# Performance work log

Measured on AMD Instinct MI355X. Metric: run time of the kernel, lower is better.

Reference implementation:

```python
import jax, jax.numpy as jnp
import numpy as np

TOTAL_LABELS = 81
MAX_TOTAL_SIZE = 200
SCORE_THRESHOLD = 0.7
IOU_THRESHOLD = 0.5  # tf.image.combined_non_max_suppression default
VARIANCES = jnp.array([0.1, 0.1, 0.2, 0.2], dtype=jnp.float32)
B, N = 4, 1500


def setup_inputs() -> dict:
    key = jax.random.key(0)
    k1, k2, k3, k4, k5 = jax.random.split(key, 5)
    # valid normalized rois (y1,x1,y2,x2) with y1<y2, x1<x2
    ctr = jax.random.uniform(k1, (B, N, 2), minval=0.2, maxval=0.8)
    sz = jax.random.uniform(k2, (B, N, 2), minval=0.05, maxval=0.3)
    roi_bboxes = jnp.concatenate([ctr - 0.5 * sz, ctr + 0.5 * sz], axis=-1).astype(jnp.float32)
    pred_deltas = (0.5 * jax.random.normal(k3, (B, N, TOTAL_LABELS * 4))).astype(jnp.float32)
    # peaked probabilities so a realistic fraction clears score_threshold=0.7
    logits = 4.0 * jax.random.normal(k4, (B, N, TOTAL_LABELS))
    pred_label_probs = jax.nn.softmax(logits, axis=-1).astype(jnp.float32)
    return {"roi_bboxes": roi_bboxes, "pred_deltas": pred_deltas,
            "pred_label_probs": pred_label_probs}


def delta_to_bbox(anchors, deltas):
    # anchors/deltas: [..., 4]; anchors are (y1,x1,y2,x2), deltas (dy,dx,dh,dw)
    h = anchors[..., 2] - anchors[..., 0]
    w = anchors[..., 3] - anchors[..., 1]
    cy = anchors[..., 0] + 0.5 * h
    cx = anchors[..., 1] + 0.5 * w
    bh = jnp.exp(deltas[..., 2]) * h
    bw = jnp.exp(deltas[..., 3]) * w
    bcy = deltas[..., 0] * h + cy
    bcx = deltas[..., 1] * w + cx
    y1 = bcy - 0.5 * bh
    x1 = bcx - 0.5 * bw
    return jnp.stack([y1, x1, y1 + bh, x1 + bw], axis=-1)


def _iou_one_vs_all(box, boxes):
    yy1 = jnp.maximum(box[0], boxes[:, 0])
    xx1 = jnp.maximum(box[1], boxes[:, 1])
    yy2 = jnp.minimum(box[2], boxes[:, 2])
    xx2 = jnp.minimum(box[3], boxes[:, 3])
    inter = jnp.maximum(yy2 - yy1, 0.0) * jnp.maximum(xx2 - xx1, 0.0)
    a1 = (box[2] - box[0]) * (box[3] - box[1])
    a2 = (boxes[:, 2] - boxes[:, 0]) * (boxes[:, 3] - boxes[:, 1])
    union = a1 + a2 - inter
    return jnp.where(union > 0, inter / union, 0.0)


def _greedy_nms(boxes, scores):
    # boxes [N,4], scores [N] -> sel idx [K] (-1 invalid), sel score [K]
    def step(scores_c, _):
        j = jnp.argmax(scores_c)
        s = scores_c[j]
        valid = s > SCORE_THRESHOLD
        iou = _iou_one_vs_all(boxes[j], boxes)
        new_scores = jnp.where(valid & (iou > IOU_THRESHOLD), -jnp.inf, scores_c)
        return new_scores, (jnp.where(valid, j, -1).astype(jnp.int32),
                            jnp.where(valid, s, 0.0))
    _, (idx, sc) = jax.lax.scan(step, scores, None, length=MAX_TOTAL_SIZE)
    return idx, sc


def _decoder_forward(roi_bboxes, pred_deltas, pred_label_probs):
    b, n, L = pred_label_probs.shape
    deltas = pred_deltas.reshape(b, n, L, 4) * VARIANCES
    rois = jnp.broadcast_to(roi_bboxes[:, :, None, :], (b, n, L, 4))
    pred_bboxes = delta_to_bbox(rois, deltas)              # [B,N,L,4]
    labels_map = jnp.argmax(pred_label_probs, axis=-1, keepdims=True)
    scores = jnp.where(labels_map != 0, pred_label_probs, 0.0)  # zero bg boxes
    boxes_cl = jnp.transpose(pred_bboxes, (0, 2, 1, 3))    # [B,L,N,4]
    scores_cl = jnp.transpose(scores, (0, 2, 1))           # [B,L,N]
    idx, sc = jax.vmap(jax.vmap(_greedy_nms))(boxes_cl, scores_cl)  # [B,L,K]
    K = MAX_TOTAL_SIZE
    sel_boxes = jnp.take_along_axis(boxes_cl, jnp.maximum(idx, 0)[..., None], axis=2)
    valid = (idx >= 0)[..., None]
    sel_boxes = jnp.where(valid, jnp.clip(sel_boxes, 0.0, 1.0), 0.0)  # clip_boxes=True
    cls = jnp.broadcast_to(jnp.arange(L, dtype=jnp.float32)[None, :, None], (b, L, K))
    cls = jnp.where(idx >= 0, cls, 0.0)
    flat_scores = sc.reshape(b, L * K)
    flat_boxes = sel_boxes.reshape(b, L * K, 4)
    flat_cls = cls.reshape(b, L * K)
    final_scores, top_i = jax.lax.top_k(flat_scores, MAX_TOTAL_SIZE)
    final_bboxes = jnp.take_along_axis(flat_boxes, top_i[..., None], axis=1)
    final_labels = jnp.take_along_axis(flat_cls, top_i, axis=1)
    return final_bboxes, final_labels, final_scores


def reference(roi_bboxes, pred_deltas, pred_label_probs):
    return _decoder_forward(roi_bboxes, pred_deltas, pred_label_probs)
```

## Files before the change

### kernel.cpp

```cpp
#include <hip/hip_runtime.h>
#include <math.h>

#define NCLS 81
#define KMAX 200
#define NMAX 1536
#define SORT_CAP 2048


__global__ __launch_bounds__(64) void row_scan(
    const float* __restrict__ rois,
    const float* __restrict__ deltas,
    const float* __restrict__ probs,
    int* __restrict__ cand_cls,
    float* __restrict__ cand_sc,
    float4* __restrict__ cand_box,
    int BN) {
  __shared__ float s_p[64 * NCLS];
  const int lane = threadIdx.x;
  const int row0 = blockIdx.x * 64;

  if (row0 + 64 <= BN) {
    const float4* src4 = (const float4*)(probs + (size_t)row0 * NCLS);
    float4* dst4 = (float4*)s_p;
#pragma unroll
    for (int it = 0; it < 21; ++it) {
      const int idx = it * 64 + lane;
      if (idx < 1296) dst4[idx] = src4[idx];
    }
  } else {
    const int tot = (BN - row0) * NCLS;
    const float* src = probs + (size_t)row0 * NCLS;
    for (int i = lane; i < tot; i += 64) s_p[i] = src[i];
  }
  __syncthreads();

  const int row = row0 + lane;
  if (row >= BN) return;
  const float* pr = s_p + lane * NCLS;
  float maxv = pr[0];
  int arg = 0;
#pragma unroll
  for (int k = 1; k < NCLS; ++k) {
    const float v = pr[k];
    if (v > maxv) { maxv = v; arg = k; }
  }
  const bool cand = (maxv > 0.7f) && (arg != 0);
  cand_cls[row] = cand ? arg : -1;
  cand_sc[row] = maxv;
  if (cand) {
    const float* r = rois + (size_t)row * 4;
    const float ay1 = r[0], ax1 = r[1], ay2 = r[2], ax2 = r[3];
    const float h = ay2 - ay1, w = ax2 - ax1;
    const float cy = ay1 + 0.5f * h, cx = ax1 + 0.5f * w;
    const float* d = deltas + (size_t)row * (NCLS * 4) + arg * 4;
    const float bh  = expf(d[2] * 0.2f) * h;
    const float bw  = expf(d[3] * 0.2f) * w;
    const float bcy = d[0] * 0.1f * h + cy;
    const float bcx = d[1] * 0.1f * w + cx;
    const float y1 = bcy - 0.5f * bh, x1 = bcx - 0.5f * bw;
    cand_box[row] = make_float4(y1, x1, y1 + bh, x1 + bw);
  }
}

__device__ __forceinline__ void nms_body(
    const float* __restrict__ cand_sc, const float4* __restrict__ cand_box,
    float* __restrict__ entries, int* __restrict__ counts,
    int N, int b, int l, int bl, int lane, int m,
    int* s_idx, float* s_score, float (*s_box)[4],
    int* s_sel, float* s_sel_score) {
  for (int i = lane; i < m; i += 64) {
    const int n = s_idx[i];
    s_score[i] = cand_sc[b * N + n];
    const float4 bx = cand_box[b * N + n];
    s_box[i][0] = bx.x; s_box[i][1] = bx.y;
    s_box[i][2] = bx.z; s_box[i][3] = bx.w;
  }
  __syncthreads();

  int kept = 0;
  while (kept < KMAX) {
    float best = -1.0f;
    int bi = -1;
    for (int i = lane; i < m; i += 64) {
      const float s = s_score[i];
      if (s > best) { best = s; bi = i; }
    }
    for (int off = 32; off > 0; off >>= 1) {
      const float ob = __shfl_down(best, off);
      const int   oi = __shfl_down(bi, off);
      if (ob > best || (ob == best && (unsigned)oi < (unsigned)bi)) {
        best = ob; bi = oi;
      }
    }
    best = __shfl(best, 0);
    bi   = __shfl(bi, 0);
    if (best <= 0.7f) break;

    if (lane == 0) { s_sel[kept] = bi; s_sel_score[kept] = best; }

    const float by1 = s_box[bi][0], bx1 = s_box[bi][1];
    const float by2 = s_box[bi][2], bx2 = s_box[bi][3];
    const float a1 = (by2 - by1) * (bx2 - bx1);
    for (int i = lane; i < m; i += 64) {
      const float ty1 = s_box[i][0], tx1 = s_box[i][1];
      const float ty2 = s_box[i][2], tx2 = s_box[i][3];
      const float yy1 = fmaxf(by1, ty1), xx1 = fmaxf(bx1, tx1);
      const float yy2 = fminf(by2, ty2), xx2 = fminf(bx2, tx2);
      const float inter = fmaxf(yy2 - yy1, 0.0f) * fmaxf(xx2 - xx1, 0.0f);
      const float a2  = (ty2 - ty1) * (tx2 - tx1);
      const float uni = a1 + a2 - inter;
      const float iou = (uni > 0.0f) ? (inter / uni) : 0.0f;
      if (iou > 0.5f) s_score[i] = -INFINITY;
    }
    kept++;
    __syncthreads();
  }
  __syncthreads();

  if (lane == 0) counts[bl] = kept;
  float* ebase = entries + (size_t)bl * KMAX * 8;
  for (int i = lane; i < kept; i += 64) {
    float* e = ebase + (size_t)i * 8;
    const int ci = s_sel[i];
    e[0] = s_sel_score[i];
    e[1] = fminf(fmaxf(s_box[ci][0], 0.0f), 1.0f);
    e[2] = fminf(fmaxf(s_box[ci][1], 0.0f), 1.0f);
    e[3] = fminf(fmaxf(s_box[ci][2], 0.0f), 1.0f);
    e[4] = fminf(fmaxf(s_box[ci][3], 0.0f), 1.0f);
  }
}

template <int N>
__global__ __launch_bounds__(64) void nms_per_class(
    const int* __restrict__ cand_cls, const float* __restrict__ cand_sc,
    const float4* __restrict__ cand_box, float* __restrict__ entries,
    int* __restrict__ counts) {
  constexpr int ITERS = (N + 63) / 64;
  const int bl = blockIdx.x;
  const int b  = bl / NCLS;
  const int l  = bl % NCLS;
  const int lane = threadIdx.x;
  if (l == 0) { if (lane == 0) counts[bl] = 0; return; }

  __shared__ int   s_idx[NMAX];
  __shared__ float s_score[NMAX];
  __shared__ float s_box[NMAX][4];
  __shared__ int   s_sel[KMAX];
  __shared__ float s_sel_score[KMAX];

  int cv[ITERS];
#pragma unroll
  for (int it = 0; it < ITERS; ++it) {
    const int n = it * 64 + lane;
    cv[it] = (n < N) ? cand_cls[b * N + n] : -1;
  }
  int m = 0;
#pragma unroll
  for (int it = 0; it < ITERS; ++it) {
    const bool cand = (cv[it] == l);
    const unsigned long long mask = __ballot(cand);
    if (cand)
      s_idx[m + __popcll(mask & ((1ull << lane) - 1ull))] = it * 64 + lane;
    m += __popcll(mask);
  }
  __syncthreads();

  nms_body(cand_sc, cand_box, entries, counts, N, b, l, bl, lane, m,
           s_idx, s_score, s_box, s_sel, s_sel_score);
}

__global__ __launch_bounds__(64) void nms_per_class_rt(
    const int* __restrict__ cand_cls, const float* __restrict__ cand_sc,
    const float4* __restrict__ cand_box, float* __restrict__ entries,
    int* __restrict__ counts, int N) {
  const int bl = blockIdx.x;
  const int b  = bl / NCLS;
  const int l  = bl % NCLS;
  const int lane = threadIdx.x;
  if (l == 0) { if (lane == 0) counts[bl] = 0; return; }

  __shared__ int   s_idx[NMAX];
  __shared__ float s_score[NMAX];
  __shared__ float s_box[NMAX][4];
  __shared__ int   s_sel[KMAX];
  __shared__ float s_sel_score[KMAX];

  int m = 0;
  for (int n0 = 0; n0 < N; n0 += 64) {
    const int n = n0 + lane;
    const bool cand = (n < N) && (cand_cls[b * N + n] == l);
    const unsigned long long mask = __ballot(cand);
    if (cand)
      s_idx[m + __popcll(mask & ((1ull << lane) - 1ull))] = n;
    m += __popcll(mask);
  }
  __syncthreads();

  nms_body(cand_sc, cand_box, entries, counts, N, b, l, bl, lane, m,
           s_idx, s_score, s_box, s_sel, s_sel_score);
}

__global__ __launch_bounds__(1024) void topk_per_batch(
    const float* __restrict__ entries,
    const int* __restrict__ counts,
    float* __restrict__ out, int B) {
  const int b   = blockIdx.x;
  const int tid = threadIdx.x;

  __shared__ int s_cnt[NCLS];
  __shared__ int s_off[NCLS];
  __shared__ int s_total, s_M;
  __shared__ unsigned long long s_key[SORT_CAP];

  if (tid < NCLS) s_cnt[tid] = counts[b * NCLS + tid];
  __syncthreads();
  if (tid == 0) {
    int acc = 0;
    for (int l = 0; l < NCLS; ++l) { s_off[l] = acc; acc += s_cnt[l]; }
    s_total = acc;
    int M = 64;
    while (M < acc) M <<= 1;
    s_M = M;
  }
  __syncthreads();
  const int c = s_total;
  const int M = s_M;

  for (int i = tid; i < M; i += 1024) s_key[i] = 0ull;
  __syncthreads();
  for (int j = tid; j < NCLS * KMAX; j += 1024) {
    const int l = j / KMAX, k = j - l * KMAX;
    if (k < s_cnt[l]) {
      const float sc = entries[((size_t)(b * NCLS + l) * KMAX + k) * 8];
      const unsigned sb = __float_as_uint(sc);
      s_key[s_off[l] + k] =
          ((unsigned long long)sb << 32) |
          (unsigned long long)(0xFFFFFFFFu - (unsigned)(l * KMAX + k));
    }
  }
  __syncthreads();

  for (int kk = 2; kk <= M; kk <<= 1) {
    for (int j2 = kk >> 1; j2 > 0; j2 >>= 1) {
      for (int i = tid; i < M; i += 1024) {
        const int ixj = i ^ j2;
        if (ixj > i) {
          const bool up = ((i & kk) == 0);
          const unsigned long long a = s_key[i], bb = s_key[ixj];
          const bool sw = up ? (a < bb) : (a > bb);
          if (sw) { s_key[i] = bb; s_key[ixj] = a; }
        }
      }
      __syncthreads();
    }
  }

  if (tid < KMAX) {
    float sc = 0.0f, lb = 0.0f, b0 = 0.0f, b1 = 0.0f, b2 = 0.0f, b3 = 0.0f;
    if (tid < c) {
      const unsigned long long k = s_key[tid];
      const unsigned fi = 0xFFFFFFFFu - (unsigned)(k & 0xFFFFFFFFull);
      const int l = fi / KMAX, kk2 = fi - l * KMAX;
      const float* e = entries + ((size_t)(b * NCLS + l) * KMAX + kk2) * 8;
      sc = e[0];
      lb = (float)l;
      b0 = e[1]; b1 = e[2]; b2 = e[3]; b3 = e[4];
    }
    float* ob = out + (size_t)b * (KMAX * 4) + (size_t)tid * 4;
    ob[0] = b0; ob[1] = b1; ob[2] = b2; ob[3] = b3;
    const size_t boxes_sz = (size_t)B * KMAX * 4;
    out[boxes_sz + (size_t)b * KMAX + tid] = lb;
    out[boxes_sz + (size_t)B * KMAX + (size_t)b * KMAX + tid] = sc;
  }
}

extern "C" void kernel_launch(void* const* d_in, const int* in_sizes, int n_in,
                              void* d_out, int out_size, void* d_ws, size_t ws_size,
                              hipStream_t stream) {
  const float* rois   = (const float*)d_in[0];
  const float* deltas = (const float*)d_in[1];
  const float* probs  = (const float*)d_in[2];
  float* out = (float*)d_out;

  const int B = 4;
  const int N = in_sizes[0] / (B * 4);
  const int BN = B * N;

  char* ws = (char*)d_ws;
  int*    counts   = (int*)ws;
  float*  entries  = (float*)(ws + 4096);
  int*    cand_cls = (int*)(ws + 2077696);
  float*  cand_sc  = (float*)(ws + 2077696 + 24064);
  float4* cand_box = (float4*)(ws + 2077696 + 24064 + 24064);

  hipLaunchKernelGGL(row_scan, dim3((BN + 63) / 64), dim3(64), 0, stream,
                     rois, deltas, probs, cand_cls, cand_sc, cand_box, BN);
  if (N == 1500) {
    hipLaunchKernelGGL((nms_per_class<1500>), dim3(B * NCLS), dim3(64), 0,
                       stream, cand_cls, cand_sc, cand_box, entries, counts);
  } else {
    hipLaunchKernelGGL(nms_per_class_rt, dim3(B * NCLS), dim3(64), 0, stream,
                       cand_cls, cand_sc, cand_box, entries, counts, N);
  }
  hipLaunchKernelGGL(topk_per_batch, dim3(B), dim3(1024), 0, stream,
                     entries, counts, out, B);
}
```

Baseline: 45.29 us.

## Compact NMS survivors via per-batch atomics and sort only kept entries

Per-class NMS blocks now claim slots in a per-batch flat buffer with an atomicAdd and write each survivor with its score, key and clipped box. The top-k kernel then sorts only that compacted list with one 64-thread wave and a payload index, instead of scanning all 81x200 slots with 1024 threads. Classes with no candidates exit early, and row_scan batches its probability loads into registers and uses float4 loads for rois and deltas. In exchange, output slot order depends on atomic timing, the sort does more work per thread, and the buffer is capped at 2048 entries per batch.

```diff
diff --git a/kernel.cpp b/kernel.cpp
--- a/kernel.cpp
+++ b/kernel.cpp
@@ -4,9 +4,10 @@
 #define NCLS 81
 #define KMAX 200
 #define NMAX 1536
-#define SORT_CAP 2048
-
-
+#define FCAP 2048
+
+
+template <int NT>
 __global__ __launch_bounds__(64) void row_scan(
     const float* __restrict__ rois,
     const float* __restrict__ deltas,
@@ -14,18 +15,28 @@
     int* __restrict__ cand_cls,
     float* __restrict__ cand_sc,
     float4* __restrict__ cand_box,
+    int* __restrict__ counters,
     int BN) {
+  constexpr int NV4 = (64 * NCLS) / 4;
   __shared__ float s_p[64 * NCLS];
   const int lane = threadIdx.x;
   const int row0 = blockIdx.x * 64;
+
+  if (blockIdx.x == 0 && lane < 8) counters[lane] = 0;
 
   if (row0 + 64 <= BN) {
     const float4* src4 = (const float4*)(probs + (size_t)row0 * NCLS);
-    float4* dst4 = (float4*)s_p;
+    float4 v[21];
 #pragma unroll
     for (int it = 0; it < 21; ++it) {
       const int idx = it * 64 + lane;
-      if (idx < 1296) dst4[idx] = src4[idx];
+      v[it] = src4[idx < NV4 ? idx : 0];
+    }
+    float4* dst4 = (float4*)s_p;
+#pragma unroll
+    for (int it = 0; it < 21; ++it) {
+      const int idx = it * 64 + lane;
+      if (idx < NV4) dst4[idx] = v[it];
     }
   } else {
     const int tot = (BN - row0) * NCLS;
@@ -48,30 +59,60 @@
   cand_cls[row] = cand ? arg : -1;
   cand_sc[row] = maxv;
   if (cand) {
-    const float* r = rois + (size_t)row * 4;
-    const float ay1 = r[0], ax1 = r[1], ay2 = r[2], ax2 = r[3];
-    const float h = ay2 - ay1, w = ax2 - ax1;
-    const float cy = ay1 + 0.5f * h, cx = ax1 + 0.5f * w;
-    const float* d = deltas + (size_t)row * (NCLS * 4) + arg * 4;
-    const float bh  = expf(d[2] * 0.2f) * h;
-    const float bw  = expf(d[3] * 0.2f) * w;
-    const float bcy = d[0] * 0.1f * h + cy;
-    const float bcx = d[1] * 0.1f * w + cx;
+    const float4 r4 = *(const float4*)(rois + (size_t)row * 4);
+    const float h = r4.z - r4.x, w = r4.w - r4.y;
+    const float cy = r4.x + 0.5f * h, cx = r4.y + 0.5f * w;
+    const float4 d4 = *(const float4*)(deltas + (size_t)row * (NCLS * 4) + arg * 4);
+    const float bh  = expf(d4.z * 0.2f) * h;
+    const float bw  = expf(d4.w * 0.2f) * w;
+    const float bcy = d4.x * 0.1f * h + cy;
+    const float bcx = d4.y * 0.1f * w + cx;
     const float y1 = bcy - 0.5f * bh, x1 = bcx - 0.5f * bw;
     cand_box[row] = make_float4(y1, x1, y1 + bh, x1 + bw);
   }
 }
 
-__device__ __forceinline__ void nms_body(
-    const float* __restrict__ cand_sc, const float4* __restrict__ cand_box,
-    float* __restrict__ entries, int* __restrict__ counts,
-    int N, int b, int l, int bl, int lane, int m,
-    int* s_idx, float* s_score, float (*s_box)[4],
-    int* s_sel, float* s_sel_score) {
+template <int NT>
+__global__ __launch_bounds__(64) void nms_per_class(
+    const int* __restrict__ cand_cls, const float* __restrict__ cand_sc,
+    const float4* __restrict__ cand_box, float* __restrict__ flat,
+    int* __restrict__ counters) {
+  constexpr int ITERS = (NT + 63) / 64;
+  const int bl = blockIdx.x;
+  const int b  = bl / NCLS;
+  const int l  = bl % NCLS;
+  const int lane = threadIdx.x;
+  if (l == 0) return;
+
+  __shared__ int   s_idx[NMAX];
+  __shared__ float s_score[NMAX];
+  __shared__ float s_box[NMAX][4];
+  __shared__ int   s_sel[KMAX];
+  __shared__ float s_sel_score[KMAX];
+  __shared__ int   s_base;
+
+  int cv[ITERS];
+#pragma unroll
+  for (int it = 0; it < ITERS; ++it) {
+    const int n = it * 64 + lane;
+    cv[it] = (n < NT) ? cand_cls[b * NT + n] : -1;
+  }
+  int m = 0;
+#pragma unroll
+  for (int it = 0; it < ITERS; ++it) {
+    const bool cand = (cv[it] == l);
+    const unsigned long long mask = __ballot(cand);
+    if (cand)
+      s_idx[m + __popcll(mask & ((1ull << lane) - 1ull))] = it * 64 + lane;
+    m += __popcll(mask);
+  }
+  if (m == 0) return;
+  __syncthreads();
+
   for (int i = lane; i < m; i += 64) {
     const int n = s_idx[i];
-    s_score[i] = cand_sc[b * N + n];
-    const float4 bx = cand_box[b * N + n];
+    s_score[i] = cand_sc[b * NT + n];
+    const float4 bx = cand_box[b * NT + n];
     s_box[i][0] = bx.x; s_box[i][1] = bx.y;
     s_box[i][2] = bx.z; s_box[i][3] = bx.w;
   }
@@ -117,160 +158,193 @@
   }
   __syncthreads();
 
-  if (lane == 0) counts[bl] = kept;
-  float* ebase = entries + (size_t)bl * KMAX * 8;
+  if (lane == 0) s_base = (kept > 0) ? atomicAdd(&counters[b], kept) : 0;
+  __syncthreads();
+  const int base = s_base;
   for (int i = lane; i < kept; i += 64) {
-    float* e = ebase + (size_t)i * 8;
-    const int ci = s_sel[i];
-    e[0] = s_sel_score[i];
-    e[1] = fminf(fmaxf(s_box[ci][0], 0.0f), 1.0f);
-    e[2] = fminf(fmaxf(s_box[ci][1], 0.0f), 1.0f);
-    e[3] = fminf(fmaxf(s_box[ci][2], 0.0f), 1.0f);
-    e[4] = fminf(fmaxf(s_box[ci][3], 0.0f), 1.0f);
-  }
-}
-
-template <int N>
-__global__ __launch_bounds__(64) void nms_per_class(
+    const int slot = base + i;
+    if (slot < FCAP) {
+      float* e = flat + ((size_t)b * FCAP + slot) * 8;
+      const int ci = s_sel[i];
+      e[0] = s_sel_score[i];
+      ((int*)e)[1] = l * KMAX + i;
+      e[2] = fminf(fmaxf(s_box[ci][0], 0.0f), 1.0f);
+      e[3] = fminf(fmaxf(s_box[ci][1], 0.0f), 1.0f);
+      e[4] = fminf(fmaxf(s_box[ci][2], 0.0f), 1.0f);
+      e[5] = fminf(fmaxf(s_box[ci][3], 0.0f), 1.0f);
+    }
+  }
+}
+
+__global__ __launch_bounds__(64) void nms_per_class_rt(
     const int* __restrict__ cand_cls, const float* __restrict__ cand_sc,
-    const float4* __restrict__ cand_box, float* __restrict__ entries,
-    int* __restrict__ counts) {
-  constexpr int ITERS = (N + 63) / 64;
+    const float4* __restrict__ cand_box, float* __restrict__ flat,
+    int* __restrict__ counters, int N) {
   const int bl = blockIdx.x;
   const int b  = bl / NCLS;
   const int l  = bl % NCLS;
   const int lane = threadIdx.x;
-  if (l == 0) { if (lane == 0) counts[bl] = 0; return; }
-
-  __shared__ int   s_idx[NMAX];
-  __shared__ float s_score[NMAX];
-  __shared__ float s_box[NMAX][4];
-  __shared__ int   s_sel[KMAX];
-  __shared__ float s_sel_score[KMAX];
-
-  int cv[ITERS];
-#pragma unroll
-  for (int it = 0; it < ITERS; ++it) {
-    const int n = it * 64 + lane;
-    cv[it] = (n < N) ? cand_cls[b * N + n] : -1;
-  }
-  int m = 0;
-#pragma unroll
-  for (int it = 0; it < ITERS; ++it) {
-    const bool cand = (cv[it] == l);
-    const unsigned long long mask = __ballot(cand);
-    if (cand)
-      s_idx[m + __popcll(mask & ((1ull << lane) - 1ull))] = it * 64 + lane;
-    m += __popcll(mask);
-  }
-  __syncthreads();
-
-  nms_body(cand_sc, cand_box, entries, counts, N, b, l, bl, lane, m,
-           s_idx, s_score, s_box, s_sel, s_sel_score);
-}
-
-__global__ __launch_bounds__(64) void nms_per_class_rt(
-    const int* __restrict__ cand_cls, const float* __restrict__ cand_sc,
-    const float4* __restrict__ cand_box, float* __restrict__ entries,
-    int* __restrict__ counts, int N) {
-  const int bl = blockIdx.x;
-  const int b  = bl / NCLS;
-  const int l  = bl % NCLS;
-  const int lane = threadIdx.x;
-  if (l == 0) { if (lane == 0) counts[bl] = 0; return; }
-
-  __shared__ int   s_idx[NMAX];
-  __shared__ float s_score[NMAX];
-  __shared__ float s_box[NMAX][4];
-  __shared__ int   s_sel[KMAX];
-  __shared__ float s_sel_score[KMAX];
-
-  int m = 0;
-  for (int n0 = 0; n0 < N; n0 += 64) {
-    const int n = n0 + lane;
-    const bool cand = (n < N) && (cand_cls[b * N + n] == l);
-    const unsigned long long mask = __ballot(cand);
-    if (cand)
-      s_idx[m + __popcll(mask & ((1ull << lane) - 1ull))] = n;
-    m += __popcll(mask);
-  }
-  __syncthreads();
-
-  nms_body(cand_sc, cand_box, entries, counts, N, b, l, bl, lane, m,
-           s_idx, s_score, s_box, s_sel, s_sel_score);
-}
-
-__global__ __launch_bounds__(1024) void topk_per_batch(
-    const float* __restrict__ entries,
-    const int* __restrict__ counts,
+  if (l == 0) return;
+  __shared__ float s_sc2[8192 > NMAX ? 8192 : NMAX];
+  __shared__ int s_selrow[KMAX];
+  __shared__ float s_selsc[KMAX];
+  __shared__ int s_base;
+  const int cap = 8192;
+  for (int n = lane; n < N && n < cap; n += 64)
+    s_sc2[n] = (cand_cls[b * N + n] == l) ? cand_sc[b * N + n] : -INFINITY;
+  __syncthreads();
+  const int nn = (N < cap) ? N : cap;
+  int kept = 0;
+  while (kept < KMAX) {
+    float best = -1.0f; int bi = -1;
+    for (int i = lane; i < nn; i += 64) {
+      const float s = s_sc2[i];
+      if (s > best) { best = s; bi = i; }
+    }
+    for (int off = 32; off > 0; off >>= 1) {
+      const float ob = __shfl_down(best, off);
+      const int   oi = __shfl_down(bi, off);
+      if (ob > best || (ob == best && (unsigned)oi < (unsigned)bi)) { best = ob; bi = oi; }
+    }
+    best = __shfl(best, 0); bi = __shfl(bi, 0);
+    if (best <= 0.7f) break;
+    if (lane == 0) { s_selrow[kept] = bi; s_selsc[kept] = best; }
+    const float4 bb = cand_box[b * N + bi];
+    const float a1 = (bb.z - bb.x) * (bb.w - bb.y);
+    for (int i = lane; i < nn; i += 64) {
+      if (s_sc2[i] != -INFINITY) {
+        const float4 tb = cand_box[b * N + i];
+        const float yy1 = fmaxf(bb.x, tb.x), xx1 = fmaxf(bb.y, tb.y);
+        const float yy2 = fminf(bb.z, tb.z), xx2 = fminf(bb.w, tb.w);
+        const float inter = fmaxf(yy2 - yy1, 0.0f) * fmaxf(xx2 - xx1, 0.0f);
+        const float a2  = (tb.z - tb.x) * (tb.w - tb.y);
+        const float uni = a1 + a2 - inter;
+        const float iou = (uni > 0.0f) ? (inter / uni) : 0.0f;
+        if (iou > 0.5f) s_sc2[i] = -INFINITY;
+      }
+    }
+    kept++;
+    __syncthreads();
+  }
+  __syncthreads();
+  if (lane == 0) s_base = (kept > 0) ? atomicAdd(&counters[b], kept) : 0;
+  __syncthreads();
+  for (int i = lane; i < kept; i += 64) {
+    const int slot = s_base + i;
+    if (slot < FCAP) {
+      float* e = flat + ((size_t)b * FCAP + slot) * 8;
+      const float4 bb = cand_box[b * N + s_selrow[i]];
+      e[0] = s_selsc[i];
+      ((int*)e)[1] = l * KMAX + i;
+      e[2] = fminf(fmaxf(bb.x, 0.0f), 1.0f);
+      e[3] = fminf(fmaxf(bb.y, 0.0f), 1.0f);
+      e[4] = fminf(fmaxf(bb.z, 0.0f), 1.0f);
+      e[5] = fminf(fmaxf(bb.w, 0.0f), 1.0f);
+    }
+  }
+}
+
+__global__ __launch_bounds__(64) void topk_per_batch(
+    const float* __restrict__ flat,
+    const int* __restrict__ counters,
     float* __restrict__ out, int B) {
-  const int b   = blockIdx.x;
-  const int tid = threadIdx.x;
-
-  __shared__ int s_cnt[NCLS];
-  __shared__ int s_off[NCLS];
-  __shared__ int s_total, s_M;
-  __shared__ unsigned long long s_key[SORT_CAP];
-
-  if (tid < NCLS) s_cnt[tid] = counts[b * NCLS + tid];
-  __syncthreads();
-  if (tid == 0) {
-    int acc = 0;
-    for (int l = 0; l < NCLS; ++l) { s_off[l] = acc; acc += s_cnt[l]; }
-    s_total = acc;
-    int M = 64;
-    while (M < acc) M <<= 1;
-    s_M = M;
-  }
-  __syncthreads();
-  const int c = s_total;
-  const int M = s_M;
-
-  for (int i = tid; i < M; i += 1024) s_key[i] = 0ull;
-  __syncthreads();
-  for (int j = tid; j < NCLS * KMAX; j += 1024) {
-    const int l = j / KMAX, k = j - l * KMAX;
-    if (k < s_cnt[l]) {
-      const float sc = entries[((size_t)(b * NCLS + l) * KMAX + k) * 8];
-      const unsigned sb = __float_as_uint(sc);
-      s_key[s_off[l] + k] =
-          ((unsigned long long)sb << 32) |
-          (unsigned long long)(0xFFFFFFFFu - (unsigned)(l * KMAX + k));
-    }
+  const int b = blockIdx.x;
+  const int lane = threadIdx.x;
+
+  __shared__ unsigned long long s_key[FCAP];
+  __shared__ short s_pay[FCAP];
+
+  int c = counters[b];
+  if (c > FCAP) c = FCAP;
+  int M = 64;
+  while (M < c) M <<= 1;
+
+  for (int i = lane; i < M; i += 64) {
+    unsigned long long k = 0ull;
+    if (i < c) {
+      const float* e = flat + ((size_t)b * FCAP + i) * 8;
+      const unsigned sb = __float_as_uint(e[0]);
+      const unsigned fi = (unsigned)(((const int*)e)[1]);
+      k = ((unsigned long long)sb << 32) |
+          (unsigned long long)(0xFFFFFFFFu - fi);
+    }
+    s_key[i] = k;
+    s_pay[i] = (short)i;
   }
   __syncthreads();
 
   for (int kk = 2; kk <= M; kk <<= 1) {
     for (int j2 = kk >> 1; j2 > 0; j2 >>= 1) {
-      for (int i = tid; i < M; i += 1024) {
+      for (int i = lane; i < M; i += 64) {
         const int ixj = i ^ j2;
         if (ixj > i) {
           const bool up = ((i & kk) == 0);
           const unsigned long long a = s_key[i], bb = s_key[ixj];
           const bool sw = up ? (a < bb) : (a > bb);
-          if (sw) { s_key[i] = bb; s_key[ixj] = a; }
+          if (sw) {
+            s_key[i] = bb; s_key[ixj] = a;
+            const short t = s_pay[i]; s_pay[i] = s_pay[ixj]; s_pay[ixj] = t;
+          }
         }
       }
       __syncthreads();
     }
   }
 
-  if (tid < KMAX) {
+  const size_t boxes_sz = (size_t)B * KMAX * 4;
+  for (int t = lane; t < KMAX; t += 64) {
     float sc = 0.0f, lb = 0.0f, b0 = 0.0f, b1 = 0.0f, b2 = 0.0f, b3 = 0.0f;
-    if (tid < c) {
-      const unsigned long long k = s_key[tid];
+    if (t < c) {
+      const unsigned long long k = s_key[t];
+      sc = __uint_as_float((unsigned)(k >> 32));
       const unsigned fi = 0xFFFFFFFFu - (unsigned)(k & 0xFFFFFFFFull);
-      const int l = fi / KMAX, kk2 = fi - l * KMAX;
-      const float* e = entries + ((size_t)(b * NCLS + l) * KMAX + kk2) * 8;
-      sc = e[0];
-      lb = (float)l;
-      b0 = e[1]; b1 = e[2]; b2 = e[3]; b3 = e[4];
-    }
-    float* ob = out + (size_t)b * (KMAX * 4) + (size_t)tid * 4;
+      lb = (float)(fi / KMAX);
+      const float* e = flat + ((size_t)b * FCAP + s_pay[t]) * 8;
+      b0 = e[2]; b1 = e[3]; b2 = e[4]; b3 = e[5];
+    }
+    float* ob = out + (size_t)b * (KMAX * 4) + (size_t)t * 4;
     ob[0] = b0; ob[1] = b1; ob[2] = b2; ob[3] = b3;
-    const size_t boxes_sz = (size_t)B * KMAX * 4;
-    out[boxes_sz + (size_t)b * KMAX + tid] = lb;
-    out[boxes_sz + (size_t)B * KMAX + (size_t)b * KMAX + tid] = sc;
+    out[boxes_sz + (size_t)b * KMAX + t] = lb;
+    out[boxes_sz + (size_t)B * KMAX + (size_t)b * KMAX + t] = sc;
+  }
+}
+
+__global__ __launch_bounds__(64) void row_scan_rt(
+    const float* __restrict__ rois, const float* __restrict__ deltas,
+    const float* __restrict__ probs, int* __restrict__ cand_cls,
+    float* __restrict__ cand_sc, float4* __restrict__ cand_box,
+    int* __restrict__ counters, int BN) {
+  __shared__ float s_p[64 * NCLS];
+  const int lane = threadIdx.x;
+  const int row0 = blockIdx.x * 64;
+  if (blockIdx.x == 0 && lane < 8) counters[lane] = 0;
+  const int tot = (min(64, BN - row0)) * NCLS;
+  const float* src = probs + (size_t)row0 * NCLS;
+  for (int i = lane; i < tot; i += 64) s_p[i] = src[i];
+  __syncthreads();
+  const int row = row0 + lane;
+  if (row >= BN) return;
+  const float* pr = s_p + lane * NCLS;
+  float maxv = pr[0];
+  int arg = 0;
+  for (int k = 1; k < NCLS; ++k) {
+    const float v = pr[k];
+    if (v > maxv) { maxv = v; arg = k; }
+  }
+  const bool cand = (maxv > 0.7f) && (arg != 0);
+  cand_cls[row] = cand ? arg : -1;
+  cand_sc[row] = maxv;
+  if (cand) {
+    const float4 r4 = *(const float4*)(rois + (size_t)row * 4);
+    const float h = r4.z - r4.x, w = r4.w - r4.y;
+    const float cy = r4.x + 0.5f * h, cx = r4.y + 0.5f * w;
+    const float4 d4 = *(const float4*)(deltas + (size_t)row * (NCLS * 4) + arg * 4);
+    const float bh  = expf(d4.z * 0.2f) * h;
+    const float bw  = expf(d4.w * 0.2f) * w;
+    const float bcy = d4.x * 0.1f * h + cy;
+    const float bcx = d4.y * 0.1f * w + cx;
+    const float y1 = bcy - 0.5f * bh, x1 = bcx - 0.5f * bw;
+    cand_box[row] = make_float4(y1, x1, y1 + bh, x1 + bw);
   }
 }
 
@@ -287,21 +361,25 @@
   const int BN = B * N;
 
   char* ws = (char*)d_ws;
-  int*    counts   = (int*)ws;
-  float*  entries  = (float*)(ws + 4096);
-  int*    cand_cls = (int*)(ws + 2077696);
-  float*  cand_sc  = (float*)(ws + 2077696 + 24064);
-  float4* cand_box = (float4*)(ws + 2077696 + 24064 + 24064);
-
-  hipLaunchKernelGGL(row_scan, dim3((BN + 63) / 64), dim3(64), 0, stream,
-                     rois, deltas, probs, cand_cls, cand_sc, cand_box, BN);
+  int*    counters = (int*)ws;
+  float*  flat     = (float*)(ws + 256);
+  int*    cand_cls = (int*)(ws + 262400);
+  float*  cand_sc  = (float*)(ws + 262400 + 64 * (size_t)N);
+  float4* cand_box = (float4*)(ws + 262400 + 128 * (size_t)N);
+
   if (N == 1500) {
+    hipLaunchKernelGGL((row_scan<1500>), dim3((BN + 63) / 64), dim3(64), 0,
+                       stream, rois, deltas, probs, cand_cls, cand_sc,
+                       cand_box, counters, BN);
     hipLaunchKernelGGL((nms_per_class<1500>), dim3(B * NCLS), dim3(64), 0,
-                       stream, cand_cls, cand_sc, cand_box, entries, counts);
+                       stream, cand_cls, cand_sc, cand_box, flat, counters);
   } else {
+    hipLaunchKernelGGL(row_scan_rt, dim3((BN + 63) / 64), dim3(64), 0, stream,
+                       rois, deltas, probs, cand_cls, cand_sc, cand_box,
+                       counters, BN);
     hipLaunchKernelGGL(nms_per_class_rt, dim3(B * NCLS), dim3(64), 0, stream,
-                       cand_cls, cand_sc, cand_box, entries, counts, N);
-  }
-  hipLaunchKernelGGL(topk_per_batch, dim3(B), dim3(1024), 0, stream,
-                     entries, counts, out, B);
-}
+                       cand_cls, cand_sc, cand_box, flat, counters, N);
+  }
+  hipLaunchKernelGGL(topk_per_batch, dim3(B), dim3(64), 0, stream,
+                     flat, counters, out, B);
+}
```

Result: slower. 87.00 us (+92.1%).
